# Kernel optimization log

Measured on AMD Instinct MI355X. Metric: run time of the kernel, lower is better.

## Reference

```python
import jax, jax.numpy as jnp
import numpy as np

NUM_CLASSES = 19
COUNT = 6
EPS = 1e-5


def setup_inputs() -> dict:
    key = jax.random.key(0)
    k1, k2 = jax.random.split(key)
    x = jax.random.normal(k1, (4, 256, 256, 256), dtype=jnp.float32)  # [B, C, H, W]
    y = jax.random.randint(k2, (4, 256, 256), 0, NUM_CLASSES)          # [B, H, W]
    return {"x": x, "y": y}


def reference(x, y):
    # Faithful vectorized version of the per-class masked mean/std loop:
    # means[b,k,c] = mean of x[b,c] over pixels with y[b]==k   (if count>COUNT else 0)
    # stds[b,k,c]  = unbiased std over those pixels + eps      (if count>COUNT else 0)
    B, C, H, W = x.shape
    N = H * W
    xf = x.reshape(B, C, N)                     # [B, C, N]
    yf = y.reshape(B, N)                        # [B, N]
    # one-hot segment membership; labels like 255 simply match no class
    onehot = (yf[:, None, :] == jnp.arange(NUM_CLASSES)[None, :, None]).astype(x.dtype)  # [B, K, N]
    cnt = onehot.sum(-1)                        # [B, K]
    s = jnp.einsum('bkn,bcn->bkc', onehot, xf)          # per-class sum
    ss = jnp.einsum('bkn,bcn->bkc', onehot, xf * xf)    # per-class sum of squares
    valid = cnt > COUNT                         # [B, K]
    vm = valid[..., None]                       # [B, K, 1]
    cnt_safe = jnp.maximum(cnt, 1.0)[..., None]
    mean = s / cnt_safe
    # unbiased variance: (sum(x^2) - n*mean^2) / (n-1)
    denom = jnp.maximum(cnt - 1.0, 1.0)[..., None]
    var = jnp.maximum((ss - cnt[..., None] * mean * mean) / denom, 0.0)
    std = jnp.sqrt(jnp.where(vm, var, 1.0)) + EPS
    means = jnp.where(vm, mean, 0.0)
    stds = jnp.where(vm, std, 0.0)
    return means, stds, valid
```

## Files before the change

### kernel.cpp

```cpp
#include <hip/hip_runtime.h>

#define NCLS 19
#define NCH 256
#define NPIX 65536
#define NBATCH 4
#define TPB 256
#define EPSV 1e-5f
#define CNT_THRESH 6
#define CSEG 16
#define SEGPIX (NPIX / CSEG)

typedef float v2f __attribute__((ext_vector_type(2)));

__global__ __launch_bounds__(TPB) void count_kernel(const int* __restrict__ y,
                                                    int* __restrict__ part) {
    const int b = blockIdx.x >> 4, seg = blockIdx.x & 15;
    const int tid = threadIdx.x, lane = tid & 63, w = tid >> 6;
    const int4* yp = (const int4*)(y + (size_t)b * NPIX + seg * SEGPIX);
    int r[NCLS];
    #pragma unroll
    for (int k = 0; k < NCLS; ++k) r[k] = 0;
    #pragma unroll
    for (int j = 0; j < 4; ++j) {
        int4 l = yp[j * TPB + tid];
        #pragma unroll
        for (int k = 0; k < NCLS; ++k)
            r[k] += (l.x == k) + (l.y == k) + (l.z == k) + (l.w == k);
    }
    __shared__ int red[4][NCLS];
    #pragma unroll
    for (int k = 0; k < NCLS; ++k) {
        int v = r[k];
        for (int off = 32; off > 0; off >>= 1) v += __shfl_down(v, off);
        if (lane == 0) red[w][k] = v;
    }
    __syncthreads();
    if (tid < NCLS)
        part[blockIdx.x * NCLS + tid] =
            red[0][tid] + red[1][tid] + red[2][tid] + red[3][tid];
}

__global__ __launch_bounds__(TPB) void moment_kernel(const float* __restrict__ x,
                                                     const int* __restrict__ y,
                                                     const int* __restrict__ part,
                                                     float* __restrict__ out) {
    const int tid = threadIdx.x, lane = tid & 63, w = tid >> 6;
    const int cp = blockIdx.x;
    const int b  = blockIdx.y;

    v2f s2[NCLS], q2[NCLS];
    #pragma unroll
    for (int k = 0; k < NCLS; ++k) { s2[k] = (v2f)0.f; q2[k] = (v2f)0.f; }

    const float4* xa = (const float4*)(x + ((size_t)(b * NCH + 2 * cp)) * NPIX);
    const float4* xb = xa + NPIX / 4;
    const int4*   yp = (const int4*)(y + (size_t)b * NPIX);

    for (int it = tid; it < NPIX / 4; it += TPB) {
        float4 va = xa[it];
        float4 vb = xb[it];
        int4   l  = yp[it];
        #pragma unroll
        for (int k = 0; k < NCLS; ++k) {
            v2f t;
            bool m;
            m = (l.x == k); t.x = m ? va.x : 0.f; t.y = m ? vb.x : 0.f;
            asm("v_pk_add_f32 %0, %0, %1" : "+v"(s2[k]) : "v"(t));
            asm("v_pk_fma_f32 %0, %1, %1, %0" : "+v"(q2[k]) : "v"(t));
            m = (l.y == k); t.x = m ? va.y : 0.f; t.y = m ? vb.y : 0.f;
            asm("v_pk_add_f32 %0, %0, %1" : "+v"(s2[k]) : "v"(t));
            asm("v_pk_fma_f32 %0, %1, %1, %0" : "+v"(q2[k]) : "v"(t));
            m = (l.z == k); t.x = m ? va.z : 0.f; t.y = m ? vb.z : 0.f;
            asm("v_pk_add_f32 %0, %0, %1" : "+v"(s2[k]) : "v"(t));
            asm("v_pk_fma_f32 %0, %1, %1, %0" : "+v"(q2[k]) : "v"(t));
            m = (l.w == k); t.x = m ? va.w : 0.f; t.y = m ? vb.w : 0.f;
            asm("v_pk_add_f32 %0, %0, %1" : "+v"(s2[k]) : "v"(t));
            asm("v_pk_fma_f32 %0, %1, %1, %0" : "+v"(q2[k]) : "v"(t));
        }
    }

    __shared__ float red[4][NCLS][4];
    #pragma unroll
    for (int k = 0; k < NCLS; ++k) {
        float sa = s2[k].x, sb = s2[k].y, qa = q2[k].x, qb = q2[k].y;
        for (int off = 32; off > 0; off >>= 1) {
            sa += __shfl_down(sa, off);
            sb += __shfl_down(sb, off);
            qa += __shfl_down(qa, off);
            qb += __shfl_down(qb, off);
        }
        if (lane == 0) { red[w][k][0] = sa; red[w][k][1] = sb; red[w][k][2] = qa; red[w][k][3] = qb; }
    }
    __syncthreads();

    if (tid < NCLS) {
        const int k = tid;
        float sa = 0.f, sb = 0.f, qa = 0.f, qb = 0.f;
        #pragma unroll
        for (int i = 0; i < 4; ++i) {
            sa += red[i][k][0]; sb += red[i][k][1];
            qa += red[i][k][2]; qb += red[i][k][3];
        }
        int n = 0;
        #pragma unroll
        for (int i = 0; i < CSEG; ++i) n += part[(b * CSEG + i) * NCLS + k];
        const float nf = (float)n;
        const bool valid = n > CNT_THRESH;
        const float inv  = 1.0f / fmaxf(nf, 1.0f);
        const float dinv = 1.0f / fmaxf(nf - 1.0f, 1.0f);
        float mean_a = sa * inv, mean_b = sb * inv;
        float var_a = fmaxf((qa - nf * mean_a * mean_a) * dinv, 0.0f);
        float var_b = fmaxf((qb - nf * mean_b * mean_b) * dinv, 0.0f);
        const int oa = (b * NCLS + k) * NCH + 2 * cp;
        out[oa]     = valid ? mean_a : 0.0f;
        out[oa + 1] = valid ? mean_b : 0.0f;
        out[NBATCH * NCLS * NCH + oa]     = valid ? (sqrtf(var_a) + EPSV) : 0.0f;
        out[NBATCH * NCLS * NCH + oa + 1] = valid ? (sqrtf(var_b) + EPSV) : 0.0f;
        if (cp == 0)
            out[2 * NBATCH * NCLS * NCH + b * NCLS + k] = valid ? 1.0f : 0.0f;
    }
}

extern "C" void kernel_launch(void* const* d_in, const int* in_sizes, int n_in,
                              void* d_out, int out_size, void* d_ws, size_t ws_size,
                              hipStream_t stream) {
    const float* x = (const float*)d_in[0];
    const int*   y = (const int*)d_in[1];
    float* out = (float*)d_out;
    int* part = (int*)d_ws;

    count_kernel<<<NBATCH * CSEG, TPB, 0, stream>>>(y, part);

    dim3 grid(NCH / 2, NBATCH);
    moment_kernel<<<grid, TPB, 0, stream>>>(x, y, part, out);
}
```

Baseline: 400.9 us.

## Replace per-class masked accumulation with LDS atomic binning and fuse counting

Instead of looping over all 19 classes per pixel with masked packed adds, each pixel is scattered into a per-lane shared-memory bin indexed by its label using LDS float atomics for sum, sum of squares and count. This removes the class-loop VALU work that dominated the kernel. Counts are now accumulated inside the moment kernel, eliminating the separate count kernel at the cost of redundant counting across channel blocks. Out-of-range labels go to an extra unused bin.

```diff
diff --git a/kernel.cpp b/kernel.cpp
--- a/kernel.cpp
+++ b/kernel.cpp
@@ -1,123 +1,95 @@
 #include <hip/hip_runtime.h>
 
 #define NCLS 19
+#define NBINS 20
 #define NCH 256
 #define NPIX 65536
 #define NBATCH 4
 #define TPB 256
 #define EPSV 1e-5f
 #define CNT_THRESH 6
-#define CSEG 16
-#define SEGPIX (NPIX / CSEG)
-
-typedef float v2f __attribute__((ext_vector_type(2)));
-
-__global__ __launch_bounds__(TPB) void count_kernel(const int* __restrict__ y,
-                                                    int* __restrict__ part) {
-    const int b = blockIdx.x >> 4, seg = blockIdx.x & 15;
-    const int tid = threadIdx.x, lane = tid & 63, w = tid >> 6;
-    const int4* yp = (const int4*)(y + (size_t)b * NPIX + seg * SEGPIX);
-    int r[NCLS];
-    #pragma unroll
-    for (int k = 0; k < NCLS; ++k) r[k] = 0;
-    #pragma unroll
-    for (int j = 0; j < 4; ++j) {
-        int4 l = yp[j * TPB + tid];
-        #pragma unroll
-        for (int k = 0; k < NCLS; ++k)
-            r[k] += (l.x == k) + (l.y == k) + (l.z == k) + (l.w == k);
-    }
-    __shared__ int red[4][NCLS];
-    #pragma unroll
-    for (int k = 0; k < NCLS; ++k) {
-        int v = r[k];
-        for (int off = 32; off > 0; off >>= 1) v += __shfl_down(v, off);
-        if (lane == 0) red[w][k] = v;
-    }
-    __syncthreads();
-    if (tid < NCLS)
-        part[blockIdx.x * NCLS + tid] =
-            red[0][tid] + red[1][tid] + red[2][tid] + red[3][tid];
-}
 
 __global__ __launch_bounds__(TPB) void moment_kernel(const float* __restrict__ x,
                                                      const int* __restrict__ y,
-                                                     const int* __restrict__ part,
                                                      float* __restrict__ out) {
     const int tid = threadIdx.x, lane = tid & 63, w = tid >> 6;
     const int cp = blockIdx.x;
     const int b  = blockIdx.y;
 
-    v2f s2[NCLS], q2[NCLS];
+    __shared__ float bins[NBINS][5][64];
+    float* bf = &bins[0][0][0];
     #pragma unroll
-    for (int k = 0; k < NCLS; ++k) { s2[k] = (v2f)0.f; q2[k] = (v2f)0.f; }
+    for (int i = tid; i < NBINS * 5 * 64; i += TPB) bf[i] = 0.f;
+    __syncthreads();
 
     const float4* xa = (const float4*)(x + ((size_t)(b * NCH + 2 * cp)) * NPIX);
     const float4* xb = xa + NPIX / 4;
     const int4*   yp = (const int4*)(y + (size_t)b * NPIX);
 
+    #pragma unroll 4
     for (int it = tid; it < NPIX / 4; it += TPB) {
         float4 va = xa[it];
         float4 vb = xb[it];
         int4   l  = yp[it];
-        #pragma unroll
-        for (int k = 0; k < NCLS; ++k) {
-            v2f t;
-            bool m;
-            m = (l.x == k); t.x = m ? va.x : 0.f; t.y = m ? vb.x : 0.f;
-            asm("v_pk_add_f32 %0, %0, %1" : "+v"(s2[k]) : "v"(t));
-            asm("v_pk_fma_f32 %0, %1, %1, %0" : "+v"(q2[k]) : "v"(t));
-            m = (l.y == k); t.x = m ? va.y : 0.f; t.y = m ? vb.y : 0.f;
-            asm("v_pk_add_f32 %0, %0, %1" : "+v"(s2[k]) : "v"(t));
-            asm("v_pk_fma_f32 %0, %1, %1, %0" : "+v"(q2[k]) : "v"(t));
-            m = (l.z == k); t.x = m ? va.z : 0.f; t.y = m ? vb.z : 0.f;
-            asm("v_pk_add_f32 %0, %0, %1" : "+v"(s2[k]) : "v"(t));
-            asm("v_pk_fma_f32 %0, %1, %1, %0" : "+v"(q2[k]) : "v"(t));
-            m = (l.w == k); t.x = m ? va.w : 0.f; t.y = m ? vb.w : 0.f;
-            asm("v_pk_add_f32 %0, %0, %1" : "+v"(s2[k]) : "v"(t));
-            asm("v_pk_fma_f32 %0, %1, %1, %0" : "+v"(q2[k]) : "v"(t));
+        {
+            unsigned c = min((unsigned)l.x, (unsigned)NCLS);
+            float* p = &bins[c][0][lane];
+            atomicAdd(p,       va.x);        atomicAdd(p + 64,  vb.x);
+            atomicAdd(p + 128, va.x * va.x); atomicAdd(p + 192, vb.x * vb.x);
+            atomicAdd(p + 256, 1.0f);
+        }
+        {
+            unsigned c = min((unsigned)l.y, (unsigned)NCLS);
+            float* p = &bins[c][0][lane];
+            atomicAdd(p,       va.y);        atomicAdd(p + 64,  vb.y);
+            atomicAdd(p + 128, va.y * va.y); atomicAdd(p + 192, vb.y * vb.y);
+            atomicAdd(p + 256, 1.0f);
+        }
+        {
+            unsigned c = min((unsigned)l.z, (unsigned)NCLS);
+            float* p = &bins[c][0][lane];
+            atomicAdd(p,       va.z);        atomicAdd(p + 64,  vb.z);
+            atomicAdd(p + 128, va.z * va.z); atomicAdd(p + 192, vb.z * vb.z);
+            atomicAdd(p + 256, 1.0f);
+        }
+        {
+            unsigned c = min((unsigned)l.w, (unsigned)NCLS);
+            float* p = &bins[c][0][lane];
+            atomicAdd(p,       va.w);        atomicAdd(p + 64,  vb.w);
+            atomicAdd(p + 128, va.w * va.w); atomicAdd(p + 192, vb.w * vb.w);
+            atomicAdd(p + 256, 1.0f);
         }
     }
+    __syncthreads();
 
-    __shared__ float red[4][NCLS][4];
-    #pragma unroll
-    for (int k = 0; k < NCLS; ++k) {
-        float sa = s2[k].x, sb = s2[k].y, qa = q2[k].x, qb = q2[k].y;
-        for (int off = 32; off > 0; off >>= 1) {
+    for (int k = w; k < NCLS; k += 4) {
+        float sa = bins[k][0][lane], sb = bins[k][1][lane],
+              qa = bins[k][2][lane], qb = bins[k][3][lane],
+              cn = bins[k][4][lane];
+        #pragma unroll
+        for (int off = 32; off; off >>= 1) {
             sa += __shfl_down(sa, off);
             sb += __shfl_down(sb, off);
             qa += __shfl_down(qa, off);
             qb += __shfl_down(qb, off);
+            cn += __shfl_down(cn, off);
         }
-        if (lane == 0) { red[w][k][0] = sa; red[w][k][1] = sb; red[w][k][2] = qa; red[w][k][3] = qb; }
-    }
-    __syncthreads();
-
-    if (tid < NCLS) {
-        const int k = tid;
-        float sa = 0.f, sb = 0.f, qa = 0.f, qb = 0.f;
-        #pragma unroll
-        for (int i = 0; i < 4; ++i) {
-            sa += red[i][k][0]; sb += red[i][k][1];
-            qa += red[i][k][2]; qb += red[i][k][3];
+        if (lane == 0) {
+            const float nf   = cn;
+            const bool  valid = nf > (float)CNT_THRESH;
+            const float inv  = 1.0f / fmaxf(nf, 1.0f);
+            const float dinv = 1.0f / fmaxf(nf - 1.0f, 1.0f);
+            const float ma = sa * inv, mb = sb * inv;
+            const float vara = fmaxf((qa - nf * ma * ma) * dinv, 0.0f);
+            const float varb = fmaxf((qb - nf * mb * mb) * dinv, 0.0f);
+            const int oa = (b * NCLS + k) * NCH + 2 * cp;
+            out[oa]     = valid ? ma : 0.0f;
+            out[oa + 1] = valid ? mb : 0.0f;
+            out[NBATCH * NCLS * NCH + oa]     = valid ? (sqrtf(vara) + EPSV) : 0.0f;
+            out[NBATCH * NCLS * NCH + oa + 1] = valid ? (sqrtf(varb) + EPSV) : 0.0f;
+            if (cp == 0)
+                out[2 * NBATCH * NCLS * NCH + b * NCLS + k] = valid ? 1.0f : 0.0f;
         }
-        int n = 0;
-        #pragma unroll
-        for (int i = 0; i < CSEG; ++i) n += part[(b * CSEG + i) * NCLS + k];
-        const float nf = (float)n;
-        const bool valid = n > CNT_THRESH;
-        const float inv  = 1.0f / fmaxf(nf, 1.0f);
-        const float dinv = 1.0f / fmaxf(nf - 1.0f, 1.0f);
-        float mean_a = sa * inv, mean_b = sb * inv;
-        float var_a = fmaxf((qa - nf * mean_a * mean_a) * dinv, 0.0f);
-        float var_b = fmaxf((qb - nf * mean_b * mean_b) * dinv, 0.0f);
-        const int oa = (b * NCLS + k) * NCH + 2 * cp;
-        out[oa]     = valid ? mean_a : 0.0f;
-        out[oa + 1] = valid ? mean_b : 0.0f;
-        out[NBATCH * NCLS * NCH + oa]     = valid ? (sqrtf(var_a) + EPSV) : 0.0f;
-        out[NBATCH * NCLS * NCH + oa + 1] = valid ? (sqrtf(var_b) + EPSV) : 0.0f;
-        if (cp == 0)
-            out[2 * NBATCH * NCLS * NCH + b * NCLS + k] = valid ? 1.0f : 0.0f;
     }
 }
 
@@ -127,10 +99,8 @@
     const float* x = (const float*)d_in[0];
     const int*   y = (const int*)d_in[1];
     float* out = (float*)d_out;
-    int* part = (int*)d_ws;
-
-    count_kernel<<<NBATCH * CSEG, TPB, 0, stream>>>(y, part);
+    (void)d_ws; (void)ws_size;
 
     dim3 grid(NCH / 2, NBATCH);
-    moment_kernel<<<grid, TPB, 0, stream>>>(x, y, part, out);
+    moment_kernel<<<grid, TPB, 0, stream>>>(x, y, out);
 }
```

Measured after the change: 1.094 ms. +172.7%, slower.
